# Optimization experiments

Measured on AMD Instinct MI355X. Metric: run time of the kernel, lower is better.

Reference implementation:

```python
import jax, jax.numpy as jnp
import numpy as np

BN_EPS = 1e-5


def grid_sample_bilinear(img, grid):
    """Torch F.grid_sample, mode=bilinear, padding_mode=zeros, align_corners=False.
    img: (B, C, H, W); grid: (B, N, 2) in [-1, 1] -> (B, C, N)."""
    B, C, H, W = img.shape
    x = ((grid[..., 0] + 1.0) * W - 1.0) * 0.5  # (B, N) pixel coords
    y = ((grid[..., 1] + 1.0) * H - 1.0) * 0.5
    x0 = jnp.floor(x)
    y0 = jnp.floor(y)
    x1 = x0 + 1.0
    y1 = y0 + 1.0
    wx1 = x - x0
    wx0 = 1.0 - wx1
    wy1 = y - y0
    wy0 = 1.0 - wy1
    img_flat = img.reshape(B, C, H * W)

    def corner(xi, yi, w):
        valid = (xi >= 0) & (xi <= W - 1) & (yi >= 0) & (yi <= H - 1)
        xi_c = jnp.clip(xi, 0, W - 1).astype(jnp.int32)
        yi_c = jnp.clip(yi, 0, H - 1).astype(jnp.int32)
        idx = yi_c * W + xi_c  # (B, N)
        vals = jnp.take_along_axis(img_flat, idx[:, None, :], axis=2)  # (B, C, N)
        return vals * (w * valid.astype(img.dtype))[:, None, :]

    return (corner(x0, y0, wx0 * wy0) + corner(x1, y0, wx1 * wy0)
            + corner(x0, y1, wx0 * wy1) + corner(x1, y1, wx1 * wy1))


def conv1x1(x, w, b):
    # x: (B, Cin, N), w: (Cout, Cin), b: (Cout,)
    return jnp.einsum('oi,bin->bon', w, x) + b[None, :, None]


def batchnorm1d_train(x, gamma, beta):
    # training-mode BN over (batch, length) per channel, biased variance
    mean = jnp.mean(x, axis=(0, 2), keepdims=True)
    var = jnp.mean((x - mean) ** 2, axis=(0, 2), keepdims=True)
    xn = (x - mean) * jax.lax.rsqrt(var + BN_EPS)
    return xn * gamma[None, :, None] + beta[None, :, None]


def setup_inputs() -> dict:
    key = jax.random.key(0)
    ks = jax.random.split(key, 12)
    B, N, CI, CP, H, W, R = 4, 16384, 256, 256, 64, 160, 4
    Cin = CI + CP
    Cb = CP // R

    def glorot(k, shape):
        fan_in = shape[1]
        return jax.random.normal(k, shape, dtype=jnp.float32) * (1.0 / np.sqrt(fan_in))

    return {
        'pts_img': jax.random.uniform(ks[0], (B, N, 2), dtype=jnp.float32, minval=-1.0, maxval=1.0),
        'img_feats': jax.random.normal(ks[1], (B, CI, H, W), dtype=jnp.float32),
        'pts_feats': jax.random.normal(ks[2], (B, CP, N), dtype=jnp.float32),
        'fusion_w': glorot(ks[3], (CP, Cin)),
        'fusion_b': jax.random.normal(ks[4], (CP,), dtype=jnp.float32) * 0.01,
        'bn_gamma': jnp.ones((CP,), dtype=jnp.float32),
        'bn_beta': jnp.zeros((CP,), dtype=jnp.float32),
        'ca1_w': glorot(ks[5], (Cb, CP)),
        'ca1_b': jax.random.normal(ks[6], (Cb,), dtype=jnp.float32) * 0.01,
        'ca2_w': glorot(ks[7], (CP, Cb)),
        'ca2_b': jax.random.normal(ks[8], (CP,), dtype=jnp.float32) * 0.01,
        'sa_w': glorot(ks[9], (Cb, CP)),
        'sa_b': jax.random.normal(ks[10], (Cb,), dtype=jnp.float32) * 0.01,
    }


def reference(pts_img, img_feats, pts_feats, fusion_w, fusion_b, bn_gamma, bn_beta,
              ca1_w, ca1_b, ca2_w, ca2_b, sa_w, sa_b):
    # grid_sample gather: (B, C_I, N)
    pts_wise_img_feats = grid_sample_bilinear(img_feats, pts_img)
    fusion = jnp.concatenate([pts_wise_img_feats, pts_feats], axis=1)  # (B, C_I+C_P, N)
    # fusion MLP: conv1x1 + BN + ReLU
    fusion = jax.nn.relu(batchnorm1d_train(conv1x1(fusion, fusion_w, fusion_b), bn_gamma, bn_beta))
    # spatial attention: max over channels of bottleneck conv, sigmoid gate
    spatial = jax.nn.sigmoid(jnp.max(conv1x1(fusion, sa_w, sa_b), axis=1, keepdims=True))
    fusion = spatial * fusion
    # channel attention: bottleneck MLP, global max-pool over points, sigmoid gate
    ca = conv1x1(jax.nn.relu(conv1x1(fusion, ca1_w, ca1_b)), ca2_w, ca2_b)  # (B, C_P, N)
    channel = jax.nn.sigmoid(jnp.max(ca, axis=2, keepdims=True))  # (B, C_P, 1)
    return channel * fusion
```

## Files before the change

### kernel.cpp

```cpp
#include <hip/hip_runtime.h>
#include <stdint.h>


typedef __attribute__((ext_vector_type(8))) short bf16x8;
typedef __attribute__((ext_vector_type(4))) float f32x4;

#define B_ 4
#define N_ 16384
#define H_ 64
#define W_ 160
#define HW_ (H_ * W_)
#define K_ 512

__device__ __forceinline__ float bf2f(unsigned short u) {
    union { unsigned int i; float f; } c; c.i = ((unsigned int)u) << 16; return c.f;
}
__device__ __forceinline__ unsigned short f2bf(float f) {
    union { float f; unsigned int i; } c; c.f = f;
    unsigned int u = c.i;
    return (unsigned short)((u + 0x7FFFu + ((u >> 16) & 1u)) >> 16);
}
__device__ __forceinline__ unsigned int fkey(float f) {
    union { float f; unsigned int u; int i; } c; c.f = f;
    return (c.i < 0) ? ~c.u : (c.u | 0x80000000u);
}
__device__ __forceinline__ float funkey(unsigned int k) {
    union { unsigned int u; float f; } c;
    c.u = (k & 0x80000000u) ? (k & 0x7FFFFFFFu) : ~k;
    return c.f;
}

__device__ __forceinline__ void async_copy16(void* lds, const void* g) {
#if defined(__has_builtin) && __has_builtin(__builtin_amdgcn_global_load_lds)
    __builtin_amdgcn_global_load_lds(
        (const __attribute__((address_space(1))) unsigned int*)g,
        (__attribute__((address_space(3))) unsigned int*)lds, 16, 0, 0);
#else
    *(uint4*)lds = *(const uint4*)g;
#endif
}

__global__ __launch_bounds__(256) void k_imgt(const float* __restrict__ img,
                                              unsigned short* __restrict__ imgT) {
    __shared__ __align__(16) unsigned short tile[64 * 68];
    int t = threadIdx.x;
    int hw0 = blockIdx.x * 64, c0 = blockIdx.y * 64, b = blockIdx.z;
    const float* src = img + ((size_t)b * 256 + c0) * HW_ + hw0;
    int sub = (t & 15) * 4, grp = t >> 4;
#pragma unroll
    for (int it = 0; it < 4; ++it) {
        int cl = grp + it * 16;
        float4 v = *(const float4*)(src + (size_t)cl * HW_ + sub);
        ushort4 o;
        o.x = f2bf(v.x); o.y = f2bf(v.y); o.z = f2bf(v.z); o.w = f2bf(v.w);
        *(ushort4*)(tile + cl * 68 + sub) = o;
    }
    __syncthreads();
    unsigned short* dst = imgT + ((size_t)b * HW_ + hw0) * 256 + c0;
#pragma unroll
    for (int it = 0; it < 4; ++it) {
        int hwl = grp + it * 16;
        ushort4 o;
        o.x = tile[(sub + 0) * 68 + hwl];
        o.y = tile[(sub + 1) * 68 + hwl];
        o.z = tile[(sub + 2) * 68 + hwl];
        o.w = tile[(sub + 3) * 68 + hwl];
        *(ushort4*)(dst + (size_t)hwl * 256 + sub) = o;
    }
}

__global__ __launch_bounds__(256) void k_xt(const float* __restrict__ pim,
                                            const unsigned short* __restrict__ imgT,
                                            const float* __restrict__ pts,
                                            unsigned short* __restrict__ XT,
                                            const float* __restrict__ fw,
                                            const float* __restrict__ saw,
                                            const float* __restrict__ c1w,
                                            const float* __restrict__ c2w,
                                            unsigned short* WfB, unsigned short* saB,
                                            unsigned short* ca1B, unsigned short* ca2B,
                                            float* buckets, unsigned int* camax) {
    __shared__ __align__(16) unsigned short tile[64 * 68];
    int t = threadIdx.x;
    int bx = blockIdx.x;
    if (bx < 4096) {
        int batch = (bx & 7) >> 1;
        int loc = (bx >> 3) * 2 + (bx & 1);
        int w = t >> 6, lane = t & 63;
        int p0 = batch * N_ + loc * 16 + w * 4;
        int c = lane * 4;
        const unsigned short* base = imgT + (size_t)batch * HW_ * 256;
        float2 g01[4];
#pragma unroll
        for (int pp = 0; pp < 4; ++pp) g01[pp] = *(const float2*)(pim + (size_t)(p0 + pp) * 2);
        ushort4 a00[4], a10[4], a01[4], a11[4];
        float w00[4], w10[4], w01[4], w11[4];
#pragma unroll
        for (int pp = 0; pp < 4; ++pp) {
            float x = (g01[pp].x + 1.0f) * (0.5f * W_) - 0.5f;
            float y = (g01[pp].y + 1.0f) * (0.5f * H_) - 0.5f;
            float xf = floorf(x), yf = floorf(y);
            float wx1 = x - xf, wx0 = 1.0f - wx1;
            float wy1 = y - yf, wy0 = 1.0f - wy1;
            int x0 = (int)xf, y0 = (int)yf;
            int x1 = x0 + 1, y1 = y0 + 1;
            float vx0 = (x0 >= 0 && x0 < W_) ? 1.f : 0.f;
            float vx1 = (x1 >= 0 && x1 < W_) ? 1.f : 0.f;
            float vy0 = (y0 >= 0 && y0 < H_) ? 1.f : 0.f;
            float vy1 = (y1 >= 0 && y1 < H_) ? 1.f : 0.f;
            int cx0 = min(max(x0, 0), W_ - 1), cx1 = min(max(x1, 0), W_ - 1);
            int cy0 = min(max(y0, 0), H_ - 1), cy1 = min(max(y1, 0), H_ - 1);
            w00[pp] = wx0 * wy0 * vx0 * vy0;
            w10[pp] = wx1 * wy0 * vx1 * vy0;
            w01[pp] = wx0 * wy1 * vx0 * vy1;
            w11[pp] = wx1 * wy1 * vx1 * vy1;
            a00[pp] = *(const ushort4*)(base + ((size_t)cy0 * W_ + cx0) * 256 + c);
            a10[pp] = *(const ushort4*)(base + ((size_t)cy0 * W_ + cx1) * 256 + c);
            a01[pp] = *(const ushort4*)(base + ((size_t)cy1 * W_ + cx0) * 256 + c);
            a11[pp] = *(const ushort4*)(base + ((size_t)cy1 * W_ + cx1) * 256 + c);
        }
#pragma unroll
        for (int pp = 0; pp < 4; ++pp) {
            ushort4 o;
            o.x = f2bf(w00[pp] * bf2f(a00[pp].x) + w10[pp] * bf2f(a10[pp].x) +
                       w01[pp] * bf2f(a01[pp].x) + w11[pp] * bf2f(a11[pp].x));
            o.y = f2bf(w00[pp] * bf2f(a00[pp].y) + w10[pp] * bf2f(a10[pp].y) +
                       w01[pp] * bf2f(a01[pp].y) + w11[pp] * bf2f(a11[pp].y));
            o.z = f2bf(w00[pp] * bf2f(a00[pp].z) + w10[pp] * bf2f(a10[pp].z) +
                       w01[pp] * bf2f(a01[pp].z) + w11[pp] * bf2f(a11[pp].z));
            o.w = f2bf(w00[pp] * bf2f(a00[pp].w) + w10[pp] * bf2f(a10[pp].w) +
                       w01[pp] * bf2f(a01[pp].w) + w11[pp] * bf2f(a11[pp].w));
            *(ushort4*)(XT + (size_t)(p0 + pp) * K_ + c) = o;
        }
    } else if (bx < 8192) {
        int j = bx - 4096;
        int n0 = (j & 255) * 64, c0 = ((j >> 8) & 3) * 64, b = j >> 10;
        const float* src = pts + ((size_t)b * 256 + c0) * N_ + n0;
        int sub = (t & 15) * 4, grp = t >> 4;
#pragma unroll
        for (int it = 0; it < 4; ++it) {
            int cl = grp + it * 16;
            float4 v = *(const float4*)(src + (size_t)cl * N_ + sub);
            ushort4 o;
            o.x = f2bf(v.x); o.y = f2bf(v.y); o.z = f2bf(v.z); o.w = f2bf(v.w);
            *(ushort4*)(tile + cl * 68 + sub) = o;
        }
        __syncthreads();
        unsigned short* dst = XT + ((size_t)b * N_ + n0) * K_ + 256 + c0;
#pragma unroll
        for (int it = 0; it < 4; ++it) {
            int nl = grp + it * 16;
            ushort4 o;
            o.x = tile[(sub + 0) * 68 + nl];
            o.y = tile[(sub + 1) * 68 + nl];
            o.z = tile[(sub + 2) * 68 + nl];
            o.w = tile[(sub + 3) * 68 + nl];
            *(ushort4*)(dst + (size_t)nl * K_ + sub) = o;
        }
    } else {
        int j = bx - 8192;
        if (j == 0) {
            for (int i = t; i < 16 * 512; i += 256) buckets[i] = 0.f;
            for (int i = t; i < 8 * 1024; i += 256) camax[i] = 0u;
        }
        int i = j * 256 + t;
        if (i < 131072) WfB[i] = f2bf(fw[i]);
        else if (i < 147456) saB[i - 131072] = f2bf(saw[i - 131072]);
        else if (i < 163840) ca1B[i - 147456] = f2bf(c1w[i - 147456]);
        else if (i < 180224) ca2B[i - 163840] = f2bf(c2w[i - 163840]);
    }
}

__global__ __launch_bounds__(256, 2) void k_gemm1(const unsigned short* __restrict__ WfB,
                                                  const unsigned short* __restrict__ XT,
                                                  const float* __restrict__ fb,
                                                  unsigned short* __restrict__ Y,
                                                  float* __restrict__ buckets) {
    __shared__ __align__(16) unsigned short At[128 * 32];
    __shared__ __align__(16) unsigned short Bt[128 * 32];
    __shared__ float biasS[128];
    __shared__ float redS[2][128], redQ[2][128];
    int t = threadIdx.x;
    int m0 = blockIdx.x * 128, n0 = blockIdx.y * 128, b = blockIdx.z;
    if (t < 128) biasS[t] = fb[m0 + t];
    const unsigned short* Xb = XT + (size_t)b * N_ * K_;
    int w = t >> 6, lane = t & 63, quad = lane >> 4, l15 = lane & 15;
    int wm = w >> 1, wn = w & 1;
    int srow = lane >> 2, scol = (lane & 3) * 8;
    const f32x4 fzero = {0.f, 0.f, 0.f, 0.f};
    f32x4 acc[4][4];
#pragma unroll
    for (int i = 0; i < 4; ++i)
#pragma unroll
        for (int j = 0; j < 4; ++j) acc[i][j] = fzero;
    for (int kt = 0; kt < 16; ++kt) {
        int k0 = kt * 32;
        __syncthreads();
#pragma unroll
        for (int cch = 0; cch < 2; ++cch) {
            int chunk = w * 2 + cch;
            int row = chunk * 16 + srow;
            async_copy16(At + chunk * 512 + lane * 8,
                         WfB + (size_t)(m0 + row) * K_ + k0 + scol);
            async_copy16(Bt + chunk * 512 + lane * 8,
                         Xb + (size_t)(n0 + row) * K_ + k0 + scol);
        }
        __syncthreads();
        bf16x8 af[4], bv[4];
#pragma unroll
        for (int i = 0; i < 4; ++i) {
            af[i] = *(const bf16x8*)(At + (wm * 64 + i * 16 + l15) * 32 + quad * 8);
            bv[i] = *(const bf16x8*)(Bt + (wn * 64 + i * 16 + l15) * 32 + quad * 8);
        }
#pragma unroll
        for (int i = 0; i < 4; ++i)
#pragma unroll
            for (int j = 0; j < 4; ++j)
                acc[i][j] = __builtin_amdgcn_mfma_f32_16x16x32_bf16(af[i], bv[j], acc[i][j], 0, 0, 0);
    }
    size_t Yb = (size_t)b * N_ * 256;
#pragma unroll
    for (int i = 0; i < 4; ++i) {
        int mloc = wm * 64 + i * 16 + quad * 4;
        float b0 = biasS[mloc + 0], b1 = biasS[mloc + 1];
        float b2 = biasS[mloc + 2], b3 = biasS[mloc + 3];
        float bb[4] = {b0, b1, b2, b3};
#pragma unroll
        for (int j = 0; j < 4; ++j) {
            int n = n0 + wn * 64 + j * 16 + l15;
            ushort4 o;
            o.x = f2bf(acc[i][j][0] + b0);
            o.y = f2bf(acc[i][j][1] + b1);
            o.z = f2bf(acc[i][j][2] + b2);
            o.w = f2bf(acc[i][j][3] + b3);
            *(ushort4*)(Y + Yb + (size_t)n * 256 + m0 + mloc) = o;
        }
#pragma unroll
        for (int r = 0; r < 4; ++r) {
            float s = 0.f, q = 0.f;
#pragma unroll
            for (int j = 0; j < 4; ++j) {
                float y = acc[i][j][r] + bb[r];
                s += y;
                q += y * y;
            }
#pragma unroll
            for (int d = 1; d < 16; d <<= 1) {
                s += __shfl_xor(s, d, 64);
                q += __shfl_xor(q, d, 64);
            }
            if (l15 == 0) {
                redS[wn][mloc + r] = s;
                redQ[wn][mloc + r] = q;
            }
        }
    }
    __syncthreads();
    if (t < 128) {
        float* bk = buckets + (size_t)(blockIdx.y & 15) * 512;
        atomicAdd(bk + m0 + t, redS[0][t] + redS[1][t]);
        atomicAdd(bk + 256 + m0 + t, redQ[0][t] + redQ[1][t]);
    }
}

__global__ __launch_bounds__(256, 2) void k_gate(const unsigned short* __restrict__ Y,
                                                 const float* __restrict__ buckets,
                                                 const float* __restrict__ gamma,
                                                 const float* __restrict__ beta,
                                                 const unsigned short* __restrict__ saB,
                                                 const float* __restrict__ sab,
                                                 const unsigned short* __restrict__ c1B,
                                                 const float* __restrict__ c1b,
                                                 const unsigned short* __restrict__ c2B,
                                                 unsigned int* __restrict__ camax,
                                                 float* __restrict__ sp_g,
                                                 float* __restrict__ ss_out) {
    __shared__ __align__(16) unsigned short Ft[64 * 264];
    __shared__ __align__(16) unsigned short Ht[64 * 72];
    __shared__ float scS[256], shS[256];
    __shared__ float saPart[4][64];
    __shared__ float spL[64];
    int t = threadIdx.x;
    size_t pts0 = (size_t)blockIdx.x * 64;
    int b = (int)(pts0 >> 14);
    int w = t >> 6, lane = t & 63, quad = lane >> 4, l15 = lane & 15;
    int jrow = w * 16 + l15;

    bf16x8 bvs[8], bvc[8];
#pragma unroll
    for (int kt = 0; kt < 8; ++kt) {
        bvs[kt] = *(const bf16x8*)(saB + (size_t)jrow * 256 + kt * 32 + quad * 8);
        bvc[kt] = *(const bf16x8*)(c1B + (size_t)jrow * 256 + kt * 32 + quad * 8);
    }
    float sbias = sab[jrow];
    float cbias = c1b[jrow];

    {
        float s = 0.f, q = 0.f;
#pragma unroll
        for (int bk = 0; bk < 16; ++bk) {
            s += buckets[bk * 512 + t];
            q += buckets[bk * 512 + 256 + t];
        }
        const float inv = 1.0f / (float)(B_ * N_);
        float mean = s * inv;
        float var = q * inv - mean * mean;
        float sc = gamma[t] * rsqrtf(var + 1e-5f);
        float sh = beta[t] - mean * sc;
        scS[t] = sc;
        shS[t] = sh;
        if (blockIdx.x == 0) { ss_out[t] = sc; ss_out[256 + t] = sh; }
    }
    __syncthreads();

    int cc = (t * 8) & 255;
    float scr[8], shr[8];
#pragma unroll
    for (int e = 0; e < 8; ++e) { scr[e] = scS[cc + e]; shr[e] = shS[cc + e]; }
    for (int idx = t * 8; idx < 64 * 256; idx += 2048) {
        int r = idx >> 8;
        uint4 v = *(const uint4*)(Y + (pts0 + r) * 256 + cc);
        unsigned short* us = (unsigned short*)&v;
#pragma unroll
        for (int e = 0; e < 8; ++e) {
            float f = bf2f(us[e]) * scr[e] + shr[e];
            us[e] = f2bf(fmaxf(f, 0.f));
        }
        *(uint4*)(Ft + r * 264 + cc) = v;
    }
    __syncthreads();

    const f32x4 fzero = {0.f, 0.f, 0.f, 0.f};
    f32x4 accS[4], accC[4];
#pragma unroll
    for (int i = 0; i < 4; ++i) { accS[i] = fzero; accC[i] = fzero; }
#pragma unroll
    for (int kt = 0; kt < 8; ++kt) {
        bf16x8 af[4];
#pragma unroll
        for (int i = 0; i < 4; ++i)
            af[i] = *(const bf16x8*)(Ft + (i * 16 + l15) * 264 + kt * 32 + quad * 8);
#pragma unroll
        for (int i = 0; i < 4; ++i) {
            accS[i] = __builtin_amdgcn_mfma_f32_16x16x32_bf16(af[i], bvs[kt], accS[i], 0, 0, 0);
            accC[i] = __builtin_amdgcn_mfma_f32_16x16x32_bf16(af[i], bvc[kt], accC[i], 0, 0, 0);
        }
    }
#pragma unroll
    for (int i = 0; i < 4; ++i) {
#pragma unroll
        for (int r = 0; r < 4; ++r) {
            float v = accS[i][r] + sbias;
#pragma unroll
            for (int d = 1; d < 16; d <<= 1) v = fmaxf(v, __shfl_xor(v, d, 64));
            if (l15 == 0) saPart[w][i * 16 + quad * 4 + r] = v;
        }
    }
    __syncthreads();
    if (t < 64) {
        float m4 = fmaxf(fmaxf(saPart[0][t], saPart[1][t]),
                         fmaxf(saPart[2][t], saPart[3][t]));
        float sv = 1.0f / (1.0f + __expf(-m4));
        spL[t] = sv;
        sp_g[pts0 + t] = sv;
    }
    __syncthreads();

#pragma unroll
    for (int i = 0; i < 4; ++i) {
#pragma unroll
        for (int r = 0; r < 4; ++r) {
            int pt = i * 16 + quad * 4 + r;
            float hv = fmaxf(accC[i][r] * spL[pt] + cbias, 0.f);
            Ht[pt * 72 + jrow] = f2bf(hv);
        }
    }
    __syncthreads();

    {
        bf16x8 b2a[4], b2b[4];
#pragma unroll
        for (int mt = 0; mt < 4; ++mt) {
            b2a[mt] = *(const bf16x8*)(c2B + (size_t)(w * 64 + mt * 16 + l15) * 64 + quad * 8);
            b2b[mt] = *(const bf16x8*)(c2B + (size_t)(w * 64 + mt * 16 + l15) * 64 + 32 + quad * 8);
        }
        float vmax[4] = {-3e38f, -3e38f, -3e38f, -3e38f};
#pragma unroll
        for (int i = 0; i < 4; ++i) {
            bf16x8 a0 = *(const bf16x8*)(Ht + (i * 16 + l15) * 72 + quad * 8);
            bf16x8 a1 = *(const bf16x8*)(Ht + (i * 16 + l15) * 72 + 32 + quad * 8);
#pragma unroll
            for (int mt = 0; mt < 4; ++mt) {
                f32x4 acc = __builtin_amdgcn_mfma_f32_16x16x32_bf16(a0, b2a[mt], fzero, 0, 0, 0);
                acc = __builtin_amdgcn_mfma_f32_16x16x32_bf16(a1, b2b[mt], acc, 0, 0, 0);
#pragma unroll
                for (int r = 0; r < 4; ++r) vmax[mt] = fmaxf(vmax[mt], acc[r]);
            }
        }
        unsigned int* cam = camax + (size_t)(blockIdx.x & 7) * 1024 + b * 256;
#pragma unroll
        for (int mt = 0; mt < 4; ++mt) {
            float v = vmax[mt];
            v = fmaxf(v, __shfl_xor(v, 16, 64));
            v = fmaxf(v, __shfl_xor(v, 32, 64));
            if (quad == 0) atomicMax(cam + w * 64 + mt * 16 + l15, fkey(v));
        }
    }
}

__global__ __launch_bounds__(256) void k_out(const unsigned short* __restrict__ Y,
                                             const unsigned int* __restrict__ camax,
                                             const float* __restrict__ c2b,
                                             const float* __restrict__ ss,
                                             const float* __restrict__ sp_g,
                                             float* __restrict__ out) {
    __shared__ __align__(16) unsigned short tile[64 * 68];
    __shared__ float ch[64], scT[64], shT[64], spT[64];
    int t = threadIdx.x;
    int n0 = blockIdx.x * 64, m0 = blockIdx.y * 64, b = blockIdx.z;
    if (t < 64) {
        int m = m0 + t;
        unsigned int k = 0u;
#pragma unroll
        for (int bk = 0; bk < 8; ++bk) k = max(k, camax[bk * 1024 + b * 256 + m]);
        ch[t] = 1.0f / (1.0f + __expf(-(funkey(k) + c2b[m])));
        scT[t] = ss[m];
        shT[t] = ss[256 + m];
        spT[t] = sp_g[(size_t)b * N_ + n0 + t];
    }
    int sub = (t & 15) * 4, grp = t >> 4;
    const unsigned short* src = Y + ((size_t)b * N_ + n0) * 256 + m0;
#pragma unroll
    for (int it = 0; it < 4; ++it) {
        int nl = grp + it * 16;
        ushort4 v = *(const ushort4*)(src + (size_t)nl * 256 + sub);
        *(ushort4*)(tile + nl * 68 + sub) = v;
    }
    __syncthreads();
    float* dst = out + ((size_t)b * 256 + m0) * N_ + n0;
#pragma unroll
    for (int it = 0; it < 4; ++it) {
        int ml = grp + it * 16;
        float g = ch[ml], scv = scT[ml], shv = shT[ml];
        float4 o;
        o.x = fmaxf(bf2f(tile[(sub + 0) * 68 + ml]) * scv + shv, 0.f) * spT[sub + 0] * g;
        o.y = fmaxf(bf2f(tile[(sub + 1) * 68 + ml]) * scv + shv, 0.f) * spT[sub + 1] * g;
        o.z = fmaxf(bf2f(tile[(sub + 2) * 68 + ml]) * scv + shv, 0.f) * spT[sub + 2] * g;
        o.w = fmaxf(bf2f(tile[(sub + 3) * 68 + ml]) * scv + shv, 0.f) * spT[sub + 3] * g;
        *(float4*)(dst + (size_t)ml * N_ + sub) = o;
    }
}

extern "C" void kernel_launch(void* const* d_in, const int* in_sizes, int n_in,
                              void* d_out, int out_size, void* d_ws, size_t ws_size,
                              hipStream_t stream) {
    (void)in_sizes; (void)n_in; (void)out_size; (void)ws_size;
    const float* pts_img = (const float*)d_in[0];
    const float* img     = (const float*)d_in[1];
    const float* pts     = (const float*)d_in[2];
    const float* fw      = (const float*)d_in[3];
    const float* fbias   = (const float*)d_in[4];
    const float* gamma   = (const float*)d_in[5];
    const float* beta    = (const float*)d_in[6];
    const float* c1w     = (const float*)d_in[7];
    const float* c1b     = (const float*)d_in[8];
    const float* c2w     = (const float*)d_in[9];
    const float* c2b     = (const float*)d_in[10];
    const float* saw     = (const float*)d_in[11];
    const float* sab     = (const float*)d_in[12];
    float* out = (float*)d_out;

    char* ws = (char*)d_ws;
    unsigned short* XT   = (unsigned short*)(ws);
    unsigned short* imgT = (unsigned short*)(ws + 67108864);
    unsigned short* Y    = (unsigned short*)(ws + 67108864);
    unsigned short* WfB  = (unsigned short*)(ws + 100663296);
    unsigned short* saB  = (unsigned short*)(ws + 100925440);
    unsigned short* ca1B = (unsigned short*)(ws + 100958208);
    unsigned short* ca2B = (unsigned short*)(ws + 100990976);
    float* buckets       = (float*)(ws + 101023744);
    unsigned int* camax  = (unsigned int*)(ws + 101056512);
    float* sp_g          = (float*)(ws + 101089280);
    float* ss            = (float*)(ws + 101351424);

    k_imgt<<<dim3(160, 4, 4), 256, 0, stream>>>(img, imgT);
    k_xt<<<8896, 256, 0, stream>>>(pts_img, imgT, pts, XT, fw, saw, c1w, c2w,
                                   WfB, saB, ca1B, ca2B, buckets, camax);
    k_gemm1<<<dim3(2, 128, 4), 256, 0, stream>>>(WfB, XT, fbias, Y, buckets);
    k_gate<<<1024, 256, 0, stream>>>(Y, buckets, gamma, beta, saB, sab, ca1B, c1b,
                                     ca2B, camax, sp_g, ss);
    k_out<<<dim3(256, 4, 4), 256, 0, stream>>>(Y, camax, c2b, ss, sp_g, out);
}
```

Baseline: 270.7 us.

## Fuse grid-sample and point-feature transpose into fusion GEMM B-tile loading

Removes the materialized XT buffer (B×N×512 bf16). The GEMM kernel now builds its B tiles directly: bilinear gather from imgT for the first half of K, and on-the-fly fp32→bf16 transpose of pts_feats for the second half. The image transpose and weight conversion are merged into one launch, and the GEMM tile becomes 256×128 so each block covers all output channels, with the Y epilogue staged through LDS for coalesced stores. This trades the XT write/read traffic and one launch for gather latency inside the GEMM main loop, no async prefetch of B, and a grid of only 512 blocks.

```diff
diff --git a/kernel.cpp b/kernel.cpp
--- a/kernel.cpp
+++ b/kernel.cpp
@@ -41,124 +41,43 @@
 }
 
 __global__ __launch_bounds__(256) void k_imgt(const float* __restrict__ img,
-                                              unsigned short* __restrict__ imgT) {
-    __shared__ __align__(16) unsigned short tile[64 * 68];
-    int t = threadIdx.x;
-    int hw0 = blockIdx.x * 64, c0 = blockIdx.y * 64, b = blockIdx.z;
-    const float* src = img + ((size_t)b * 256 + c0) * HW_ + hw0;
-    int sub = (t & 15) * 4, grp = t >> 4;
-#pragma unroll
-    for (int it = 0; it < 4; ++it) {
-        int cl = grp + it * 16;
-        float4 v = *(const float4*)(src + (size_t)cl * HW_ + sub);
-        ushort4 o;
-        o.x = f2bf(v.x); o.y = f2bf(v.y); o.z = f2bf(v.z); o.w = f2bf(v.w);
-        *(ushort4*)(tile + cl * 68 + sub) = o;
-    }
-    __syncthreads();
-    unsigned short* dst = imgT + ((size_t)b * HW_ + hw0) * 256 + c0;
-#pragma unroll
-    for (int it = 0; it < 4; ++it) {
-        int hwl = grp + it * 16;
-        ushort4 o;
-        o.x = tile[(sub + 0) * 68 + hwl];
-        o.y = tile[(sub + 1) * 68 + hwl];
-        o.z = tile[(sub + 2) * 68 + hwl];
-        o.w = tile[(sub + 3) * 68 + hwl];
-        *(ushort4*)(dst + (size_t)hwl * 256 + sub) = o;
-    }
-}
-
-__global__ __launch_bounds__(256) void k_xt(const float* __restrict__ pim,
-                                            const unsigned short* __restrict__ imgT,
-                                            const float* __restrict__ pts,
-                                            unsigned short* __restrict__ XT,
-                                            const float* __restrict__ fw,
-                                            const float* __restrict__ saw,
-                                            const float* __restrict__ c1w,
-                                            const float* __restrict__ c2w,
-                                            unsigned short* WfB, unsigned short* saB,
-                                            unsigned short* ca1B, unsigned short* ca2B,
-                                            float* buckets, unsigned int* camax) {
-    __shared__ __align__(16) unsigned short tile[64 * 68];
+                                              unsigned short* __restrict__ imgT,
+                                              const float* __restrict__ fw,
+                                              const float* __restrict__ saw,
+                                              const float* __restrict__ c1w,
+                                              const float* __restrict__ c2w,
+                                              unsigned short* WfB, unsigned short* saB,
+                                              unsigned short* ca1B, unsigned short* ca2B,
+                                              float* buckets, unsigned int* camax) {
     int t = threadIdx.x;
     int bx = blockIdx.x;
-    if (bx < 4096) {
-        int batch = (bx & 7) >> 1;
-        int loc = (bx >> 3) * 2 + (bx & 1);
-        int w = t >> 6, lane = t & 63;
-        int p0 = batch * N_ + loc * 16 + w * 4;
-        int c = lane * 4;
-        const unsigned short* base = imgT + (size_t)batch * HW_ * 256;
-        float2 g01[4];
-#pragma unroll
-        for (int pp = 0; pp < 4; ++pp) g01[pp] = *(const float2*)(pim + (size_t)(p0 + pp) * 2);
-        ushort4 a00[4], a10[4], a01[4], a11[4];
-        float w00[4], w10[4], w01[4], w11[4];
-#pragma unroll
-        for (int pp = 0; pp < 4; ++pp) {
-            float x = (g01[pp].x + 1.0f) * (0.5f * W_) - 0.5f;
-            float y = (g01[pp].y + 1.0f) * (0.5f * H_) - 0.5f;
-            float xf = floorf(x), yf = floorf(y);
-            float wx1 = x - xf, wx0 = 1.0f - wx1;
-            float wy1 = y - yf, wy0 = 1.0f - wy1;
-            int x0 = (int)xf, y0 = (int)yf;
-            int x1 = x0 + 1, y1 = y0 + 1;
-            float vx0 = (x0 >= 0 && x0 < W_) ? 1.f : 0.f;
-            float vx1 = (x1 >= 0 && x1 < W_) ? 1.f : 0.f;
-            float vy0 = (y0 >= 0 && y0 < H_) ? 1.f : 0.f;
-            float vy1 = (y1 >= 0 && y1 < H_) ? 1.f : 0.f;
-            int cx0 = min(max(x0, 0), W_ - 1), cx1 = min(max(x1, 0), W_ - 1);
-            int cy0 = min(max(y0, 0), H_ - 1), cy1 = min(max(y1, 0), H_ - 1);
-            w00[pp] = wx0 * wy0 * vx0 * vy0;
-            w10[pp] = wx1 * wy0 * vx1 * vy0;
-            w01[pp] = wx0 * wy1 * vx0 * vy1;
-            w11[pp] = wx1 * wy1 * vx1 * vy1;
-            a00[pp] = *(const ushort4*)(base + ((size_t)cy0 * W_ + cx0) * 256 + c);
-            a10[pp] = *(const ushort4*)(base + ((size_t)cy0 * W_ + cx1) * 256 + c);
-            a01[pp] = *(const ushort4*)(base + ((size_t)cy1 * W_ + cx0) * 256 + c);
-            a11[pp] = *(const ushort4*)(base + ((size_t)cy1 * W_ + cx1) * 256 + c);
-        }
-#pragma unroll
-        for (int pp = 0; pp < 4; ++pp) {
-            ushort4 o;
-            o.x = f2bf(w00[pp] * bf2f(a00[pp].x) + w10[pp] * bf2f(a10[pp].x) +
-                       w01[pp] * bf2f(a01[pp].x) + w11[pp] * bf2f(a11[pp].x));
-            o.y = f2bf(w00[pp] * bf2f(a00[pp].y) + w10[pp] * bf2f(a10[pp].y) +
-                       w01[pp] * bf2f(a01[pp].y) + w11[pp] * bf2f(a11[pp].y));
-            o.z = f2bf(w00[pp] * bf2f(a00[pp].z) + w10[pp] * bf2f(a10[pp].z) +
-                       w01[pp] * bf2f(a01[pp].z) + w11[pp] * bf2f(a11[pp].z));
-            o.w = f2bf(w00[pp] * bf2f(a00[pp].w) + w10[pp] * bf2f(a10[pp].w) +
-                       w01[pp] * bf2f(a01[pp].w) + w11[pp] * bf2f(a11[pp].w));
-            *(ushort4*)(XT + (size_t)(p0 + pp) * K_ + c) = o;
-        }
-    } else if (bx < 8192) {
-        int j = bx - 4096;
-        int n0 = (j & 255) * 64, c0 = ((j >> 8) & 3) * 64, b = j >> 10;
-        const float* src = pts + ((size_t)b * 256 + c0) * N_ + n0;
+    if (bx < 2560) {
+        __shared__ __align__(16) unsigned short tile[64 * 68];
+        int hw0 = (bx % 160) * 64, c0 = ((bx / 160) & 3) * 64, b = bx / 640;
+        const float* src = img + ((size_t)b * 256 + c0) * HW_ + hw0;
         int sub = (t & 15) * 4, grp = t >> 4;
 #pragma unroll
         for (int it = 0; it < 4; ++it) {
             int cl = grp + it * 16;
-            float4 v = *(const float4*)(src + (size_t)cl * N_ + sub);
+            float4 v = *(const float4*)(src + (size_t)cl * HW_ + sub);
             ushort4 o;
             o.x = f2bf(v.x); o.y = f2bf(v.y); o.z = f2bf(v.z); o.w = f2bf(v.w);
             *(ushort4*)(tile + cl * 68 + sub) = o;
         }
         __syncthreads();
-        unsigned short* dst = XT + ((size_t)b * N_ + n0) * K_ + 256 + c0;
+        unsigned short* dst = imgT + ((size_t)b * HW_ + hw0) * 256 + c0;
 #pragma unroll
         for (int it = 0; it < 4; ++it) {
-            int nl = grp + it * 16;
+            int hwl = grp + it * 16;
             ushort4 o;
-            o.x = tile[(sub + 0) * 68 + nl];
-            o.y = tile[(sub + 1) * 68 + nl];
-            o.z = tile[(sub + 2) * 68 + nl];
-            o.w = tile[(sub + 3) * 68 + nl];
-            *(ushort4*)(dst + (size_t)nl * K_ + sub) = o;
+            o.x = tile[(sub + 0) * 68 + hwl];
+            o.y = tile[(sub + 1) * 68 + hwl];
+            o.z = tile[(sub + 2) * 68 + hwl];
+            o.w = tile[(sub + 3) * 68 + hwl];
+            *(ushort4*)(dst + (size_t)hwl * 256 + sub) = o;
         }
     } else {
-        int j = bx - 8192;
+        int j = bx - 2560;
         if (j == 0) {
             for (int i = t; i < 16 * 512; i += 256) buckets[i] = 0.f;
             for (int i = t; i < 8 * 1024; i += 256) camax[i] = 0u;
@@ -171,95 +90,190 @@
     }
 }
 
-__global__ __launch_bounds__(256, 2) void k_gemm1(const unsigned short* __restrict__ WfB,
-                                                  const unsigned short* __restrict__ XT,
-                                                  const float* __restrict__ fb,
-                                                  unsigned short* __restrict__ Y,
-                                                  float* __restrict__ buckets) {
-    __shared__ __align__(16) unsigned short At[128 * 32];
-    __shared__ __align__(16) unsigned short Bt[128 * 32];
-    __shared__ float biasS[128];
-    __shared__ float redS[2][128], redQ[2][128];
+__global__ __launch_bounds__(256, 2) void k_gemm1f(const unsigned short* __restrict__ WfB,
+                                                   const float* __restrict__ pim,
+                                                   const unsigned short* __restrict__ imgT,
+                                                   const float* __restrict__ pts,
+                                                   const float* __restrict__ fb,
+                                                   unsigned short* __restrict__ Y,
+                                                   float* __restrict__ buckets) {
+    __shared__ __align__(16) char smem[37888];
+    unsigned short* At = (unsigned short*)smem;
+    unsigned short* Bt = (unsigned short*)(smem + 16384);
+    uint4*  offs4 = (uint4*)(smem + 26624);
+    float4* wts4  = (float4*)(smem + 28672);
+    unsigned short* tile = (unsigned short*)smem;
+    float* biasS = (float*)(smem + 34816);
+    float* redS  = (float*)(smem + 35840);
+    float* redQ  = (float*)(smem + 36864);
+
     int t = threadIdx.x;
-    int m0 = blockIdx.x * 128, n0 = blockIdx.y * 128, b = blockIdx.z;
-    if (t < 128) biasS[t] = fb[m0 + t];
-    const unsigned short* Xb = XT + (size_t)b * N_ * K_;
+    int n0 = blockIdx.x * 128, bb = blockIdx.y;
     int w = t >> 6, lane = t & 63, quad = lane >> 4, l15 = lane & 15;
-    int wm = w >> 1, wn = w & 1;
-    int srow = lane >> 2, scol = (lane & 3) * 8;
+    const unsigned short* imb = imgT + (size_t)bb * HW_ * 256;
+
+    if (t < 128) {
+        float2 g2 = *(const float2*)(pim + (size_t)((size_t)bb * N_ + n0 + t) * 2);
+        float x = (g2.x + 1.0f) * (0.5f * W_) - 0.5f;
+        float y = (g2.y + 1.0f) * (0.5f * H_) - 0.5f;
+        float xf = floorf(x), yf = floorf(y);
+        float wx1 = x - xf, wx0 = 1.0f - wx1;
+        float wy1 = y - yf, wy0 = 1.0f - wy1;
+        int x0 = (int)xf, y0 = (int)yf;
+        int x1 = x0 + 1, y1 = y0 + 1;
+        float vx0 = (x0 >= 0 && x0 < W_) ? 1.f : 0.f;
+        float vx1 = (x1 >= 0 && x1 < W_) ? 1.f : 0.f;
+        float vy0 = (y0 >= 0 && y0 < H_) ? 1.f : 0.f;
+        float vy1 = (y1 >= 0 && y1 < H_) ? 1.f : 0.f;
+        int cx0 = min(max(x0, 0), W_ - 1), cx1 = min(max(x1, 0), W_ - 1);
+        int cy0 = min(max(y0, 0), H_ - 1), cy1 = min(max(y1, 0), H_ - 1);
+        uint4 o4;
+        o4.x = (unsigned)(cy0 * W_ + cx0);
+        o4.y = (unsigned)(cy0 * W_ + cx1);
+        o4.z = (unsigned)(cy1 * W_ + cx0);
+        o4.w = (unsigned)(cy1 * W_ + cx1);
+        offs4[t] = o4;
+        float4 w4;
+        w4.x = wx0 * wy0 * vx0 * vy0;
+        w4.y = wx1 * wy0 * vx1 * vy0;
+        w4.z = wx0 * wy1 * vx0 * vy1;
+        w4.w = wx1 * wy1 * vx1 * vy1;
+        wts4[t] = w4;
+    }
+
     const f32x4 fzero = {0.f, 0.f, 0.f, 0.f};
-    f32x4 acc[4][4];
+    f32x4 acc[4][8];
 #pragma unroll
     for (int i = 0; i < 4; ++i)
 #pragma unroll
-        for (int j = 0; j < 4; ++j) acc[i][j] = fzero;
+        for (int j = 0; j < 8; ++j) acc[i][j] = fzero;
+
     for (int kt = 0; kt < 16; ++kt) {
         int k0 = kt * 32;
         __syncthreads();
 #pragma unroll
-        for (int cch = 0; cch < 2; ++cch) {
-            int chunk = w * 2 + cch;
-            int row = chunk * 16 + srow;
-            async_copy16(At + chunk * 512 + lane * 8,
-                         WfB + (size_t)(m0 + row) * K_ + k0 + scol);
-            async_copy16(Bt + chunk * 512 + lane * 8,
-                         Xb + (size_t)(n0 + row) * K_ + k0 + scol);
+        for (int q = 0; q < 4; ++q) {
+            int row = q * 64 + (t >> 2);
+            async_copy16(At + (size_t)q * 2048 + (size_t)t * 8,
+                         WfB + (size_t)row * K_ + k0 + (t & 3) * 8);
+        }
+        if (kt < 8) {
+#pragma unroll
+            for (int pass = 0; pass < 2; ++pass) {
+                int tau = pass * 256 + t;
+                int pt = tau >> 2, cg = tau & 3;
+                uint4 o4 = offs4[pt];
+                float4 w4 = wts4[pt];
+                int ch = k0 + cg * 8;
+                uint4 cA = *(const uint4*)(imb + (size_t)o4.x * 256 + ch);
+                uint4 cB = *(const uint4*)(imb + (size_t)o4.y * 256 + ch);
+                uint4 cC = *(const uint4*)(imb + (size_t)o4.z * 256 + ch);
+                uint4 cD = *(const uint4*)(imb + (size_t)o4.w * 256 + ch);
+                const unsigned short* pa = (const unsigned short*)&cA;
+                const unsigned short* pb = (const unsigned short*)&cB;
+                const unsigned short* pc = (const unsigned short*)&cC;
+                const unsigned short* pd = (const unsigned short*)&cD;
+                uint4 ov;
+                unsigned short* po = (unsigned short*)&ov;
+#pragma unroll
+                for (int e = 0; e < 8; ++e)
+                    po[e] = f2bf(w4.x * bf2f(pa[e]) + w4.y * bf2f(pb[e]) +
+                                 w4.z * bf2f(pc[e]) + w4.w * bf2f(pd[e]));
+                *(uint4*)(Bt + pt * 40 + cg * 8) = ov;
+            }
+        } else {
+            int c_local = t & 31, g = t >> 5;
+            int c = (kt - 8) * 32 + c_local;
+            const float* src = pts + ((size_t)bb * 256 + c) * (size_t)N_ + n0 + g * 16;
+            float4 v0 = *(const float4*)(src + 0);
+            float4 v1 = *(const float4*)(src + 4);
+            float4 v2 = *(const float4*)(src + 8);
+            float4 v3 = *(const float4*)(src + 12);
+            unsigned short* dst = Bt + (size_t)g * 16 * 40 + c_local;
+            dst[0 * 40] = f2bf(v0.x); dst[1 * 40] = f2bf(v0.y);
+            dst[2 * 40] = f2bf(v0.z); dst[3 * 40] = f2bf(v0.w);
+            dst[4 * 40] = f2bf(v1.x); dst[5 * 40] = f2bf(v1.y);
+            dst[6 * 40] = f2bf(v1.z); dst[7 * 40] = f2bf(v1.w);
+            dst[8 * 40] = f2bf(v2.x); dst[9 * 40] = f2bf(v2.y);
+            dst[10 * 40] = f2bf(v2.z); dst[11 * 40] = f2bf(v2.w);
+            dst[12 * 40] = f2bf(v3.x); dst[13 * 40] = f2bf(v3.y);
+            dst[14 * 40] = f2bf(v3.z); dst[15 * 40] = f2bf(v3.w);
         }
         __syncthreads();
-        bf16x8 af[4], bv[4];
-#pragma unroll
-        for (int i = 0; i < 4; ++i) {
-            af[i] = *(const bf16x8*)(At + (wm * 64 + i * 16 + l15) * 32 + quad * 8);
-            bv[i] = *(const bf16x8*)(Bt + (wn * 64 + i * 16 + l15) * 32 + quad * 8);
-        }
+        bf16x8 af[4], bv[8];
+#pragma unroll
+        for (int j = 0; j < 8; ++j)
+            bv[j] = *(const bf16x8*)(Bt + (j * 16 + l15) * 40 + quad * 8);
 #pragma unroll
         for (int i = 0; i < 4; ++i)
-#pragma unroll
-            for (int j = 0; j < 4; ++j)
+            af[i] = *(const bf16x8*)(At + (w * 64 + i * 16 + l15) * 32 + quad * 8);
+#pragma unroll
+        for (int i = 0; i < 4; ++i)
+#pragma unroll
+            for (int j = 0; j < 8; ++j)
                 acc[i][j] = __builtin_amdgcn_mfma_f32_16x16x32_bf16(af[i], bv[j], acc[i][j], 0, 0, 0);
     }
-    size_t Yb = (size_t)b * N_ * 256;
+
+    __syncthreads();
+    biasS[t] = fb[t];
+    __syncthreads();
 #pragma unroll
     for (int i = 0; i < 4; ++i) {
-        int mloc = wm * 64 + i * 16 + quad * 4;
-        float b0 = biasS[mloc + 0], b1 = biasS[mloc + 1];
-        float b2 = biasS[mloc + 2], b3 = biasS[mloc + 3];
-        float bb[4] = {b0, b1, b2, b3};
-#pragma unroll
-        for (int j = 0; j < 4; ++j) {
-            int n = n0 + wn * 64 + j * 16 + l15;
-            ushort4 o;
-            o.x = f2bf(acc[i][j][0] + b0);
-            o.y = f2bf(acc[i][j][1] + b1);
-            o.z = f2bf(acc[i][j][2] + b2);
-            o.w = f2bf(acc[i][j][3] + b3);
-            *(ushort4*)(Y + Yb + (size_t)n * 256 + m0 + mloc) = o;
-        }
+        int mq = w * 64 + i * 16 + quad * 4;
 #pragma unroll
         for (int r = 0; r < 4; ++r) {
+            float bia = biasS[mq + r];
             float s = 0.f, q = 0.f;
 #pragma unroll
-            for (int j = 0; j < 4; ++j) {
-                float y = acc[i][j][r] + bb[r];
-                s += y;
-                q += y * y;
+            for (int j = 0; j < 8; ++j) {
+                float y = acc[i][j][r] + bia;
+                s += y; q += y * y;
             }
 #pragma unroll
             for (int d = 1; d < 16; d <<= 1) {
                 s += __shfl_xor(s, d, 64);
                 q += __shfl_xor(q, d, 64);
             }
-            if (l15 == 0) {
-                redS[wn][mloc + r] = s;
-                redQ[wn][mloc + r] = q;
+            if (l15 == 0) { redS[mq + r] = s; redQ[mq + r] = q; }
+        }
+    }
+    size_t Yrow0 = ((size_t)bb * N_ + n0) * 256;
+#pragma unroll
+    for (int h = 0; h < 2; ++h) {
+        if (h == 1) __syncthreads();
+        if ((w >> 1) == h) {
+            int hw = w & 1;
+#pragma unroll
+            for (int i = 0; i < 4; ++i) {
+                int mloc = hw * 64 + i * 16 + quad * 4;
+                int mg = h * 128 + mloc;
+                float b0 = biasS[mg + 0], b1 = biasS[mg + 1];
+                float b2 = biasS[mg + 2], b3 = biasS[mg + 3];
+#pragma unroll
+                for (int j = 0; j < 8; ++j) {
+                    int n = j * 16 + l15;
+                    ushort4 o;
+                    o.x = f2bf(acc[i][j][0] + b0);
+                    o.y = f2bf(acc[i][j][1] + b1);
+                    o.z = f2bf(acc[i][j][2] + b2);
+                    o.w = f2bf(acc[i][j][3] + b3);
+                    *(ushort4*)(tile + n * 136 + mloc) = o;
+                }
             }
         }
-    }
-    __syncthreads();
-    if (t < 128) {
-        float* bk = buckets + (size_t)(blockIdx.y & 15) * 512;
-        atomicAdd(bk + m0 + t, redS[0][t] + redS[1][t]);
-        atomicAdd(bk + 256 + m0 + t, redQ[0][t] + redQ[1][t]);
+        __syncthreads();
+        if (h == 0) {
+            float* bk = buckets + (size_t)(blockIdx.x & 15) * 512;
+            atomicAdd(bk + t, redS[t]);
+            atomicAdd(bk + 256 + t, redQ[t]);
+        }
+#pragma unroll
+        for (int pass = 0; pass < 8; ++pass) {
+            int row = pass * 16 + (t >> 4);
+            int cB = (t & 15) * 8;
+            uint4 v = *(const uint4*)(tile + row * 136 + cB);
+            *(uint4*)(Y + Yrow0 + (size_t)row * 256 + h * 128 + cB) = v;
+        }
     }
 }
 
@@ -471,22 +485,20 @@
     float* out = (float*)d_out;
 
     char* ws = (char*)d_ws;
-    unsigned short* XT   = (unsigned short*)(ws);
-    unsigned short* imgT = (unsigned short*)(ws + 67108864);
-    unsigned short* Y    = (unsigned short*)(ws + 67108864);
-    unsigned short* WfB  = (unsigned short*)(ws + 100663296);
-    unsigned short* saB  = (unsigned short*)(ws + 100925440);
-    unsigned short* ca1B = (unsigned short*)(ws + 100958208);
-    unsigned short* ca2B = (unsigned short*)(ws + 100990976);
-    float* buckets       = (float*)(ws + 101023744);
-    unsigned int* camax  = (unsigned int*)(ws + 101056512);
-    float* sp_g          = (float*)(ws + 101089280);
-    float* ss            = (float*)(ws + 101351424);
-
-    k_imgt<<<dim3(160, 4, 4), 256, 0, stream>>>(img, imgT);
-    k_xt<<<8896, 256, 0, stream>>>(pts_img, imgT, pts, XT, fw, saw, c1w, c2w,
-                                   WfB, saB, ca1B, ca2B, buckets, camax);
-    k_gemm1<<<dim3(2, 128, 4), 256, 0, stream>>>(WfB, XT, fbias, Y, buckets);
+    unsigned short* imgT = (unsigned short*)(ws);
+    unsigned short* Y    = (unsigned short*)(ws + 20971520);
+    unsigned short* WfB  = (unsigned short*)(ws + 54525952);
+    unsigned short* saB  = (unsigned short*)(ws + 54788096);
+    unsigned short* ca1B = (unsigned short*)(ws + 54820864);
+    unsigned short* ca2B = (unsigned short*)(ws + 54853632);
+    float* buckets       = (float*)(ws + 54886400);
+    unsigned int* camax  = (unsigned int*)(ws + 54919168);
+    float* sp_g          = (float*)(ws + 54951936);
+    float* ss            = (float*)(ws + 55214080);
+
+    k_imgt<<<3264, 256, 0, stream>>>(img, imgT, fw, saw, c1w, c2w,
+                                     WfB, saB, ca1B, ca2B, buckets, camax);
+    k_gemm1f<<<dim3(128, 4), 256, 0, stream>>>(WfB, pts_img, imgT, pts, fbias, Y, buckets);
     k_gate<<<1024, 256, 0, stream>>>(Y, buckets, gamma, beta, saB, sab, ca1B, c1b,
                                      ca2B, camax, sp_g, ss);
     k_out<<<dim3(256, 4, 4), 256, 0, stream>>>(Y, camax, c2b, ss, sp_g, out);
```

New measurement: 245.2 us. 1.1x faster.
